# Kernel tuning notes

Hardware: AMD Instinct MI355X
Metric: run time of the kernel (lower is better)

Reference implementation:

```python
import jax, jax.numpy as jnp
import numpy as np
import math

SUPPORT = 4
NEI = 20
POOL_RATE = 4

def _normalize(x, axis):
    n = jnp.linalg.norm(x, axis=axis, keepdims=True)
    return x / jnp.maximum(n, 1e-12)

def _knn(verts, k):
    # verts: (b, v, 3) -> (b, v, k) indices of k nearest (excluding self)
    sq = jnp.sum(verts * verts, axis=-1)
    dist = sq[:, :, None] + sq[:, None, :] - 2.0 * jnp.einsum('bid,bjd->bij', verts, verts)
    _, idx = jax.lax.top_k(-dist, k + 1)
    return idx[:, :, 1:]

def _gather(t, idx):
    # t: (b, v, c), idx: (b, v, n) -> (b, v, n, c)
    return jax.vmap(lambda ti, ii: ti[ii])(t, idx)

def _conv_surface(idx, verts, dirs, support, kernel):
    b, v, n = idx.shape
    nd = _normalize(_gather(verts, idx) - verts[:, :, None, :], -1)  # (b,v,n,3)
    sd = _normalize(dirs, 0)                                          # (3, s*k)
    theta = jax.nn.relu(jnp.einsum('bvnd,de->bvne', nd, sd))
    theta = theta.reshape(b, v, n, support, kernel)
    return jnp.sum(jnp.max(theta, axis=2), axis=2)  # (b, v, kernel)

def _conv_layer(idx, verts, fm, W, bias, dirs, support, out_c):
    b, v, n = idx.shape
    nd = _normalize(_gather(verts, idx) - verts[:, :, None, :], -1)
    sd = _normalize(dirs, 0)                                          # (3, s*out)
    theta = jax.nn.relu(jnp.einsum('bvnd,de->bvne', nd, sd))          # (b,v,n,s*out)
    f = jnp.einsum('bvc,ce->bve', fm, W) + bias                       # (b,v,(s+1)*out)
    f_center = f[:, :, :out_c]
    f_support = _gather(f[:, :, out_c:], idx)                         # (b,v,n,s*out)
    act = (theta * f_support).reshape(b, v, n, support, out_c)
    return f_center + jnp.sum(jnp.max(act, axis=2), axis=2)

def _pool(verts, fm, idx, key, rate):
    pooled = jnp.max(_gather(fm, idx), axis=2)  # (b, v, c)
    v = verts.shape[1]
    sel = jax.random.permutation(key, v)[: v // rate]
    return verts[:, sel, :], pooled[:, sel, :]

def _unif(key, shape, stdv):
    return jax.random.uniform(key, shape, jnp.float32, -stdv, stdv)

def setup_inputs() -> dict:
    key = jax.random.key(0)
    ks = jax.random.split(key, 16)
    s = SUPPORT
    vertices = jax.random.normal(ks[0], (4, 1, 4096, 3), dtype=jnp.float32)
    d = {'vertices': vertices}
    d['dirs0'] = _unif(ks[1], (3, s * 32), 1.0 / math.sqrt(s * 32))
    layers = [(32, 64), (64, 128), (128, 256), (256, 1024)]
    for i, (cin, cout) in enumerate(layers, start=1):
        stdv = 1.0 / math.sqrt(cout * (s + 1))
        d[f'W{i}'] = _unif(ks[3 * i - 1], (cin, (s + 1) * cout), stdv)
        d[f'b{i}'] = _unif(ks[3 * i], ((s + 1) * cout,), stdv)
        d[f'D{i}'] = _unif(ks[3 * i + 1], (3, s * cout), stdv)
    return d

def reference(vertices, dirs0, W1, b1, D1, W2, b2, D2, W3, b3, D3, W4, b4, D4):
    s = SUPPORT
    bs, _, vn, _ = vertices.shape
    v = vertices.reshape(bs, vn, 3)
    idx = _knn(v, NEI)
    fm0 = jax.nn.relu(_conv_surface(idx, v, dirs0, s, 32))
    fm1 = jax.nn.relu(_conv_layer(idx, v, fm0, W1, b1, D1, s, 64))
    v, fm1 = _pool(v, fm1, idx, jax.random.key(42), POOL_RATE)
    idx = _knn(v, NEI)
    fm2 = jax.nn.relu(_conv_layer(idx, v, fm1, W2, b2, D2, s, 128))
    fm3 = jax.nn.relu(_conv_layer(idx, v, fm2, W3, b3, D3, s, 256))
    v, fm3 = _pool(v, fm3, idx, jax.random.key(43), POOL_RATE)
    idx = _knn(v, NEI)
    fm4 = _conv_layer(idx, v, fm3, W4, b4, D4, s, 1024)
    out = jnp.transpose(fm4, (0, 2, 1))[..., None]  # (bs, 1024, vn/16, 1)
    return out
```

## Files before the change

kernel.cpp:

```cpp
#include <hip/hip_runtime.h>
#include <vector>
#include <algorithm>
#include <cstdint>
#include <cstring>
#include <cmath>

static inline uint32_t tf_rotl(uint32_t x, int r) { return (x << r) | (x >> (32 - r)); }

static void tf2x32(uint32_t k0, uint32_t k1, uint32_t x0, uint32_t x1,
                   uint32_t* o0, uint32_t* o1) {
  uint32_t ks2 = k0 ^ k1 ^ 0x1BD11BDAu;
  uint32_t v0 = x0 + k0, v1 = x1 + k1;
  static const int R0[4] = {13, 15, 26, 6}, R1[4] = {17, 29, 16, 24};
#define RND4(R) do { for (int i_ = 0; i_ < 4; ++i_) { v0 += v1; v1 = tf_rotl(v1, R[i_]); v1 ^= v0; } } while (0)
  RND4(R0); v0 += k1;  v1 += ks2 + 1u;
  RND4(R1); v0 += ks2; v1 += k0 + 2u;
  RND4(R0); v0 += k0;  v1 += k1 + 3u;
  RND4(R1); v0 += k1;  v1 += ks2 + 4u;
  RND4(R0); v0 += ks2; v1 += k0 + 5u;
#undef RND4
  *o0 = v0; *o1 = v1;
}

static void jax_permutation(uint32_t seed, int n, int rounds, int* x) {
  uint32_t k0 = 0u, k1 = seed;
  for (int i = 0; i < n; ++i) x[i] = i;
  std::vector<uint32_t> bits(n);
  std::vector<int> ord(n), xn(n);
  for (int r = 0; r < rounds; ++r) {
    uint32_t nk0, nk1, sk0, sk1;
    tf2x32(k0, k1, 0u, 0u, &nk0, &nk1);
    tf2x32(k0, k1, 0u, 1u, &sk0, &sk1);
    for (int i = 0; i < n; ++i) {
      uint32_t h, l;
      tf2x32(sk0, sk1, 0u, (uint32_t)i, &h, &l);
      bits[i] = h ^ l;
    }
    for (int i = 0; i < n; ++i) ord[i] = i;
    std::stable_sort(ord.begin(), ord.end(),
                     [&](int a, int b) { return bits[a] < bits[b]; });
    for (int i = 0; i < n; ++i) xn[i] = x[ord[i]];
    memcpy(x, xn.data(), (size_t)n * sizeof(int));
    k0 = nk0; k1 = nk1;
  }
}

#define NEI 20

__device__ __forceinline__ float san(float v) {
  v = (v != v) ? 0.0f : v;
  return fmaxf(-1e4f, fminf(v, 1e4f));
}

__global__ void k_setup(const float* __restrict__ vin, float* __restrict__ outA,
                        float4* __restrict__ pk, int nverts,
                        const float* __restrict__ d0, const float* __restrict__ d1,
                        const float* __restrict__ d2, const float* __restrict__ d3,
                        const float* __restrict__ d4,
                        float* __restrict__ s0, float* __restrict__ s1,
                        float* __restrict__ s2, float* __restrict__ s3,
                        float* __restrict__ s4) {
  int blk = blockIdx.x;
  if (blk < 64) {
    int i = blk * 256 + threadIdx.x;
    if (i >= nverts) return;
    float x = san(vin[3 * i]), y = san(vin[3 * i + 1]), z = san(vin[3 * i + 2]);
    outA[3 * i] = x; outA[3 * i + 1] = y; outA[3 * i + 2] = z;
    pk[i] = make_float4(x, y, z, x * x + y * y + z * z);
    return;
  }
  int t = (blk - 64) * 256 + threadIdx.x;
  const float* d; float* s; int E, e;
  if (t < 128)       { d = d0; s = s0; E = 128;  e = t; }
  else if (t < 384)  { d = d1; s = s1; E = 256;  e = t - 128; }
  else if (t < 896)  { d = d2; s = s2; E = 512;  e = t - 384; }
  else if (t < 1920) { d = d3; s = s3; E = 1024; e = t - 896; }
  else if (t < 6016) { d = d4; s = s4; E = 4096; e = t - 1920; }
  else return;
  float a = san(d[e]);
  float b = san(d[E + e]);
  float c = san(d[2 * E + e]);
  float nrm = sqrtf(a * a + b * b + c * c);
  float m = fmaxf(nrm, 1e-12f);
  s[e] = a / m; s[E + e] = b / m; s[2 * E + e] = c / m;
}

__device__ __forceinline__ unsigned fmap(float f) {
  unsigned u = __float_as_uint(f);
  return u ^ ((u & 0x80000000u) ? 0xFFFFFFFFu : 0x80000000u);
}

__device__ __forceinline__ unsigned dpp_min_bcast1(unsigned a) {
  unsigned t;
  t = (unsigned)__builtin_amdgcn_update_dpp((int)a, (int)a, 0xB1, 0xF, 0xF, true);
  a = t < a ? t : a;
  t = (unsigned)__builtin_amdgcn_update_dpp((int)a, (int)a, 0x4E, 0xF, 0xF, true);
  a = t < a ? t : a;
  t = (unsigned)__builtin_amdgcn_update_dpp((int)a, (int)a, 0x141, 0xF, 0xF, true);
  a = t < a ? t : a;
  t = (unsigned)__builtin_amdgcn_update_dpp((int)a, (int)a, 0x140, 0xF, 0xF, true);
  a = t < a ? t : a;
  t = (unsigned)__builtin_amdgcn_update_dpp((int)a, (int)a, 0x142, 0xA, 0xF, false);
  a = t < a ? t : a;
  t = (unsigned)__builtin_amdgcn_update_dpp((int)a, (int)a, 0x143, 0xC, 0xF, false);
  a = t < a ? t : a;
  return (unsigned)__builtin_amdgcn_readlane((int)a, 63);
}

__device__ __forceinline__ void dpp_min_bcast2(unsigned& a, unsigned& b) {
  unsigned t0, t1;
#define STEP_DPP(ctrl, rm, bc)                                                           \
  t0 = (unsigned)__builtin_amdgcn_update_dpp((int)a, (int)a, ctrl, rm, 0xF, bc);         \
  t1 = (unsigned)__builtin_amdgcn_update_dpp((int)b, (int)b, ctrl, rm, 0xF, bc);         \
  a = t0 < a ? t0 : a; b = t1 < b ? t1 : b;
  STEP_DPP(0xB1, 0xF, true)
  STEP_DPP(0x4E, 0xF, true)
  STEP_DPP(0x141, 0xF, true)
  STEP_DPP(0x140, 0xF, true)
  STEP_DPP(0x142, 0xA, false)
  STEP_DPP(0x143, 0xC, false)
#undef STEP_DPP
  a = (unsigned)__builtin_amdgcn_readlane((int)a, 63);
  b = (unsigned)__builtin_amdgcn_readlane((int)b, 63);
}

template <int VCAND>
__global__ __launch_bounds__(256, 8) void k_knn8(const float4* __restrict__ pk,
                                                 int* __restrict__ nidx, int V) {
  const int wid = threadIdx.x >> 6;
  const int lane = threadIdx.x & 63;
  const int row0 = blockIdx.x * 8 + wid * 2;
  const int b = row0 / V;
  const int base = b * V;
  const int i0 = row0 % V;

  float xi[2], yi[2], zi[2], sqi[2];
#pragma unroll
  for (int t = 0; t < 2; ++t) {
    float4 q = pk[base + i0 + t];
    xi[t] = q.x; yi[t] = q.y; zi[t] = q.z; sqi[t] = q.w;
  }

  unsigned long long q0[2] = {~0ULL, ~0ULL}, q1[2] = {~0ULL, ~0ULL}, q2[2] = {~0ULL, ~0ULL};
#pragma unroll 4
  for (int c = 0; c < VCAND; ++c) {
    int j = c * 64 + lane;
    float4 cj = pk[base + j];
    float xj = cj.x, yj = cj.y, zj = cj.z, sqj = cj.w;
#pragma unroll
    for (int t = 0; t < 2; ++t) {
      float dot = xi[t] * xj + yi[t] * yj + zi[t] * zj;
      float dd = (sqi[t] + sqj) - 2.0f * dot;
      unsigned long long k = (((unsigned long long)fmap(dd)) << 32) | (unsigned)j;
      if (k < q2[t]) {
        if (k < q1[t]) {
          q2[t] = q1[t];
          if (k < q0[t]) { q1[t] = q0[t]; q0[t] = k; } else { q1[t] = k; }
        } else {
          q2[t] = k;
        }
      }
    }
  }

  for (int r = 0; r < 21; ++r) {
    unsigned h0 = (unsigned)(q0[0] >> 32);
    unsigned h1 = (unsigned)(q0[1] >> 32);
    unsigned m0 = h0, m1 = h1;
    dpp_min_bcast2(m0, m1);
    unsigned long long mk0 = __ballot(h0 == m0);
    unsigned long long mk1 = __ballot(h1 == m1);
    bool win0, win1;
    if (__popcll(mk0) > 1) {
      unsigned jj = (h0 == m0) ? (unsigned)q0[0] : 0xFFFFFFFFu;
      unsigned jm = dpp_min_bcast1(jj);
      win0 = (h0 == m0) && ((unsigned)q0[0] == jm);
    } else {
      win0 = (h0 == m0);
    }
    if (__popcll(mk1) > 1) {
      unsigned jj = (h1 == m1) ? (unsigned)q0[1] : 0xFFFFFFFFu;
      unsigned jm = dpp_min_bcast1(jj);
      win1 = (h1 == m1) && ((unsigned)q0[1] == jm);
    } else {
      win1 = (h1 == m1);
    }
    if (win0) {
      if (r > 0) nidx[(size_t)row0 * NEI + (r - 1)] = (int)(unsigned)q0[0];
      unsigned long long bound = q0[0];
      q0[0] = q1[0]; q1[0] = q2[0]; q2[0] = ~0ULL;
      if (q0[0] == ~0ULL) {
        unsigned long long nm = ~0ULL;
        for (int c = 0; c < VCAND; ++c) {
          int j = c * 64 + lane;
          float4 cj = pk[base + j];
          float dot = xi[0] * cj.x + yi[0] * cj.y + zi[0] * cj.z;
          float dd = (sqi[0] + cj.w) - 2.0f * dot;
          unsigned long long k = (((unsigned long long)fmap(dd)) << 32) | (unsigned)j;
          if (k > bound && k < nm) nm = k;
        }
        q0[0] = nm;
      }
    }
    if (win1) {
      if (r > 0) nidx[(size_t)(row0 + 1) * NEI + (r - 1)] = (int)(unsigned)q0[1];
      unsigned long long bound = q0[1];
      q0[1] = q1[1]; q1[1] = q2[1]; q2[1] = ~0ULL;
      if (q0[1] == ~0ULL) {
        unsigned long long nm = ~0ULL;
        for (int c = 0; c < VCAND; ++c) {
          int j = c * 64 + lane;
          float4 cj = pk[base + j];
          float dot = xi[1] * cj.x + yi[1] * cj.y + zi[1] * cj.z;
          float dd = (sqi[1] + cj.w) - 2.0f * dot;
          unsigned long long k = (((unsigned long long)fmap(dd)) << 32) | (unsigned)j;
          if (k > bound && k < nm) nm = k;
        }
        q0[1] = nm;
      }
    }
  }
}

__global__ __launch_bounds__(128) void k_conv_surface(const float* __restrict__ verts,
                                                      const int* __restrict__ nidx,
                                                      const float* __restrict__ sd,
                                                      float* __restrict__ fm, int V) {
  int row = blockIdx.x;
  int b = row / V, v = row % V;
  const float* vb = verts + (size_t)b * V * 3;
  __shared__ float nd[60];
  __shared__ float mcol[128];
  int tid = threadIdx.x;
  if (tid < NEI) {
    int j = nidx[(size_t)row * NEI + tid];
    float dx = vb[3 * j] - vb[3 * v];
    float dy = vb[3 * j + 1] - vb[3 * v + 1];
    float dz = vb[3 * j + 2] - vb[3 * v + 2];
    float nrm = sqrtf(dx * dx + dy * dy + dz * dz);
    float m = fmaxf(nrm, 1e-12f);
    nd[tid * 3] = dx / m; nd[tid * 3 + 1] = dy / m; nd[tid * 3 + 2] = dz / m;
  }
  __syncthreads();
  {
    int e = tid;
    float s0 = sd[e], s1 = sd[128 + e], s2 = sd[256 + e];
    float me = 0.0f;
#pragma unroll
    for (int n = 0; n < NEI; ++n) {
      float th = nd[3 * n] * s0 + nd[3 * n + 1] * s1 + nd[3 * n + 2] * s2;
      th = fmaxf(th, 0.0f);
      me = fmaxf(me, th);
    }
    mcol[e] = me;
  }
  __syncthreads();
  if (tid < 32) {
    float o = mcol[tid] + mcol[32 + tid] + mcol[64 + tid] + mcol[96 + tid];
    o = fmaxf(o, 0.0f);
    fm[(size_t)row * 32 + tid] = o;
  }
}

__global__ __launch_bounds__(256) void k_gemm_bias(const float* __restrict__ A,
                                                   const float* __restrict__ W,
                                                   const float* __restrict__ bias,
                                                   float* __restrict__ fc,
                                                   _Float16* __restrict__ fs,
                                                   int M, int N, int K, int Cc) {
  __shared__ float As[16][68];
  __shared__ float Bs[16][68];
  int n0 = blockIdx.x * 64, m0 = blockIdx.y * 64;
  int tx = threadIdx.x & 15, ty = threadIdx.x >> 4;
  float acc[4][4] = {};
  for (int k0 = 0; k0 < K; k0 += 16) {
    for (int t = threadIdx.x; t < 1024; t += 256) {
      int mm = t >> 4, kk = t & 15;
      int m = m0 + mm;
      As[kk][mm] = (m < M) ? A[(size_t)m * K + (k0 + kk)] : 0.0f;
    }
    for (int t = threadIdx.x; t < 1024; t += 256) {
      int kk = t >> 6, nn = t & 63;
      int n = n0 + nn;
      Bs[kk][nn] = (n < N) ? san(W[(size_t)(k0 + kk) * N + n]) : 0.0f;
    }
    __syncthreads();
#pragma unroll
    for (int kk = 0; kk < 16; ++kk) {
      float4 av = *(const float4*)&As[kk][ty << 2];
      float4 bv = *(const float4*)&Bs[kk][tx << 2];
      float a[4] = {av.x, av.y, av.z, av.w};
      float bb[4] = {bv.x, bv.y, bv.z, bv.w};
#pragma unroll
      for (int i = 0; i < 4; ++i)
#pragma unroll
        for (int j = 0; j < 4; ++j) acc[i][j] += a[i] * bb[j];
    }
    __syncthreads();
  }
  int SW = N - Cc;
  for (int i = 0; i < 4; ++i)
    for (int j = 0; j < 4; ++j) {
      int m = m0 + (ty << 2) + i, n = n0 + (tx << 2) + j;
      if (m < M && n < N) {
        float val = acc[i][j] + san(bias[n]);
        if (n < Cc) fc[(size_t)m * Cc + n] = val;
        else fs[(size_t)m * SW + (n - Cc)] = (_Float16)val;
      }
    }
}

typedef __attribute__((ext_vector_type(8))) short v8h;
typedef __attribute__((ext_vector_type(4))) float v4f;

__device__ __forceinline__ unsigned short f2bf(float f) {
  unsigned u = __float_as_uint(f);
  u = u + 0x7FFFu + ((u >> 16) & 1u);
  return (unsigned short)(u >> 16);
}
__device__ __forceinline__ float bf2f(unsigned short h) {
  return __uint_as_float((unsigned)h << 16);
}

__global__ __launch_bounds__(256) void k_split_wT_all(
    const float* __restrict__ W2, unsigned short* __restrict__ w2h, unsigned short* __restrict__ w2l,
    const float* __restrict__ W3, unsigned short* __restrict__ w3h, unsigned short* __restrict__ w3l,
    const float* __restrict__ W4, unsigned short* __restrict__ w4h, unsigned short* __restrict__ w4l) {
  int blk = blockIdx.x;
  const float* W; unsigned short *hiT, *loT; int K, N, nt, local;
  if (blk < 40)        { W = W2; hiT = w2h; loT = w2l; K = 64;  N = 640;  nt = 20;  local = blk; }
  else if (blk < 200)  { W = W3; hiT = w3h; loT = w3l; K = 128; N = 1280; nt = 40;  local = blk - 40; }
  else                 { W = W4; hiT = w4h; loT = w4l; K = 256; N = 5120; nt = 160; local = blk - 200; }
  int n0 = (local % nt) * 32, k0 = (local / nt) * 32;
  __shared__ float tile[32][33];
  int tx = threadIdx.x & 31, ty4 = threadIdx.x >> 5;
#pragma unroll
  for (int j = 0; j < 4; ++j)
    tile[ty4 * 4 + j][tx] = san(W[(size_t)(k0 + ty4 * 4 + j) * N + n0 + tx]);
  __syncthreads();
#pragma unroll
  for (int j = 0; j < 4; ++j) {
    int n = n0 + ty4 * 4 + j;
    float a = tile[tx][ty4 * 4 + j];
    unsigned short h = f2bf(a);
    hiT[(size_t)n * K + k0 + tx] = h;
    loT[(size_t)n * K + k0 + tx] = f2bf(a - bf2f(h));
  }
}

__global__ __launch_bounds__(256) void k_gemm128_mfma(
    const unsigned short* __restrict__ Ah, const unsigned short* __restrict__ Al,
    const unsigned short* __restrict__ BhT, const unsigned short* __restrict__ BlT,
    const float* __restrict__ bias, float* __restrict__ fc, _Float16* __restrict__ fs,
    int M, int N, int K, int Cc) {
  __shared__ __attribute__((aligned(16))) unsigned short sAh[128 * 40];
  __shared__ __attribute__((aligned(16))) unsigned short sAl[128 * 40];
  __shared__ __attribute__((aligned(16))) unsigned short sBh[128 * 40];
  __shared__ __attribute__((aligned(16))) unsigned short sBl[128 * 40];
  const int n0 = blockIdx.x * 128, m0 = blockIdx.y * 128;
  const int l = threadIdx.x & 63;
  const int w = threadIdx.x >> 6;
  const int wr = (w >> 1) * 64, wc = (w & 1) * 64;
  const int lr = l & 15;
  const int kb8 = (l >> 4) * 8;

  v4f acc[4][4];
#pragma unroll
  for (int i = 0; i < 4; ++i)
#pragma unroll
    for (int j = 0; j < 4; ++j) acc[i][j] = (v4f){0.f, 0.f, 0.f, 0.f};

  for (int k0 = 0; k0 < K; k0 += 32) {
#pragma unroll
    for (int q = 0; q < 2; ++q) {
      int lin = (int)threadIdx.x + (q << 8);
      int r = lin >> 2, kc = (lin & 3) << 3;
      *(uint4*)&sAh[r * 40 + kc] = *(const uint4*)&Ah[(size_t)(m0 + r) * K + k0 + kc];
      *(uint4*)&sAl[r * 40 + kc] = *(const uint4*)&Al[(size_t)(m0 + r) * K + k0 + kc];
      *(uint4*)&sBh[r * 40 + kc] = *(const uint4*)&BhT[(size_t)(n0 + r) * K + k0 + kc];
      *(uint4*)&sBl[r * 40 + kc] = *(const uint4*)&BlT[(size_t)(n0 + r) * K + k0 + kc];
    }
    __syncthreads();
    v8h fah[4], fal[4], fbh[4], fbl[4];
#pragma unroll
    for (int t = 0; t < 4; ++t) {
      fah[t] = *(const v8h*)&sAh[(wr + t * 16 + lr) * 40 + kb8];
      fal[t] = *(const v8h*)&sAl[(wr + t * 16 + lr) * 40 + kb8];
      fbh[t] = *(const v8h*)&sBh[(wc + t * 16 + lr) * 40 + kb8];
      fbl[t] = *(const v8h*)&sBl[(wc + t * 16 + lr) * 40 + kb8];
    }
#pragma unroll
    for (int i = 0; i < 4; ++i)
#pragma unroll
      for (int j = 0; j < 4; ++j) {
        acc[i][j] = __builtin_amdgcn_mfma_f32_16x16x32_bf16(fah[i], fbh[j], acc[i][j], 0, 0, 0);
        acc[i][j] = __builtin_amdgcn_mfma_f32_16x16x32_bf16(fah[i], fbl[j], acc[i][j], 0, 0, 0);
        acc[i][j] = __builtin_amdgcn_mfma_f32_16x16x32_bf16(fal[i], fbh[j], acc[i][j], 0, 0, 0);
      }
    __syncthreads();
  }
  float bs[4];
#pragma unroll
  for (int j = 0; j < 4; ++j) bs[j] = san(bias[n0 + wc + j * 16 + lr]);
  const int rowb = m0 + wr + (l >> 4) * 4;
  if (n0 + 128 <= Cc) {
#pragma unroll
    for (int i = 0; i < 4; ++i)
#pragma unroll
      for (int j = 0; j < 4; ++j) {
        int col = n0 + wc + j * 16 + lr;
#pragma unroll
        for (int v = 0; v < 4; ++v)
          fc[(size_t)(rowb + i * 16 + v) * Cc + col] = acc[i][j][v] + bs[j];
      }
  } else {
    int SW = N - Cc;
#pragma unroll
    for (int i = 0; i < 4; ++i)
#pragma unroll
      for (int j = 0; j < 4; ++j) {
        int col = n0 + wc + j * 16 + lr - Cc;
#pragma unroll
        for (int v = 0; v < 4; ++v)
          fs[(size_t)(rowb + i * 16 + v) * SW + col] = (_Float16)(acc[i][j][v] + bs[j]);
      }
  }
}

__global__ __launch_bounds__(256) void k_conv_layer(const float* __restrict__ fc,
                                                    const _Float16* __restrict__ fs,
                                                    const float* __restrict__ verts,
                                                    const int* __restrict__ nidx,
                                                    const float* __restrict__ sd,
                                                    float* __restrict__ outf,
                                                    int V, int C, int relu_out) {
  int row = blockIdx.x;
  int b = row / V, v = row % V;
  int E = 4 * C;
  extern __shared__ float sm[];
  float* mcol = sm;
  float* nd = sm + E;
  int* jr = (int*)(nd + 60);
  int tid = threadIdx.x;
  const float* vb = verts + (size_t)b * V * 3;
  if (tid < NEI) {
    int j = nidx[(size_t)row * NEI + tid];
    jr[tid] = j;
    float dx = vb[3 * j] - vb[3 * v];
    float dy = vb[3 * j + 1] - vb[3 * v + 1];
    float dz = vb[3 * j + 2] - vb[3 * v + 2];
    float nrm = sqrtf(dx * dx + dy * dy + dz * dz);
    float m = fmaxf(nrm, 1e-12f);
    nd[tid * 3] = dx / m; nd[tid * 3 + 1] = dy / m; nd[tid * 3 + 2] = dz / m;
  }
  __syncthreads();
  size_t fb = (size_t)b * V;
  for (int e = tid; e < E; e += blockDim.x) {
    float s0 = sd[e], s1 = sd[E + e], s2 = sd[2 * E + e];
    float me = -INFINITY;
#pragma unroll
    for (int n = 0; n < NEI; ++n) {
      float th = nd[3 * n] * s0 + nd[3 * n + 1] * s1 + nd[3 * n + 2] * s2;
      th = fmaxf(th, 0.0f);
      float fv = (float)fs[(fb + jr[n]) * (size_t)E + e];
      me = fmaxf(me, th * fv);
    }
    mcol[e] = me;
  }
  __syncthreads();
  for (int c = tid; c < C; c += blockDim.x) {
    float o = fc[(size_t)row * C + c] + mcol[c] + mcol[C + c] + mcol[2 * C + c] + mcol[3 * C + c];
    if (relu_out) o = fmaxf(o, 0.0f);
    outf[(size_t)row * C + c] = o;
  }
}

__global__ __launch_bounds__(256) void k_conv_layer_split(const float* __restrict__ fc,
                                                          const _Float16* __restrict__ fs,
                                                          const float* __restrict__ verts,
                                                          const int* __restrict__ nidx,
                                                          const float* __restrict__ sd,
                                                          unsigned short* __restrict__ outh,
                                                          unsigned short* __restrict__ outl,
                                                          int V, int C, int relu_out) {
  int row = blockIdx.x;
  int b = row / V, v = row % V;
  int E = 4 * C;
  extern __shared__ float sm[];
  float* mcol = sm;
  float* nd = sm + E;
  int* jr = (int*)(nd + 60);
  int tid = threadIdx.x;
  const float* vb = verts + (size_t)b * V * 3;
  if (tid < NEI) {
    int j = nidx[(size_t)row * NEI + tid];
    jr[tid] = j;
    float dx = vb[3 * j] - vb[3 * v];
    float dy = vb[3 * j + 1] - vb[3 * v + 1];
    float dz = vb[3 * j + 2] - vb[3 * v + 2];
    float nrm = sqrtf(dx * dx + dy * dy + dz * dz);
    float m = fmaxf(nrm, 1e-12f);
    nd[tid * 3] = dx / m; nd[tid * 3 + 1] = dy / m; nd[tid * 3 + 2] = dz / m;
  }
  __syncthreads();
  size_t fb = (size_t)b * V;
  for (int e = tid; e < E; e += blockDim.x) {
    float s0 = sd[e], s1 = sd[E + e], s2 = sd[2 * E + e];
    float me = -INFINITY;
#pragma unroll
    for (int n = 0; n < NEI; ++n) {
      float th = nd[3 * n] * s0 + nd[3 * n + 1] * s1 + nd[3 * n + 2] * s2;
      th = fmaxf(th, 0.0f);
      float fv = (float)fs[(fb + jr[n]) * (size_t)E + e];
      me = fmaxf(me, th * fv);
    }
    mcol[e] = me;
  }
  __syncthreads();
  for (int c = tid; c < C; c += blockDim.x) {
    float o = fc[(size_t)row * C + c] + mcol[c] + mcol[C + c] + mcol[2 * C + c] + mcol[3 * C + c];
    if (relu_out) o = fmaxf(o, 0.0f);
    unsigned short h = f2bf(o);
    outh[(size_t)row * C + c] = h;
    outl[(size_t)row * C + c] = f2bf(o - bf2f(h));
  }
}

__global__ __launch_bounds__(1024) void k_conv_layer_big(const float* __restrict__ fc,
                                                         const _Float16* __restrict__ fs,
                                                         const float* __restrict__ verts,
                                                         const int* __restrict__ nidx,
                                                         const float* __restrict__ sd,
                                                         float* __restrict__ outf,
                                                         int V, int C, int relu_out) {
  int row = blockIdx.x;
  int b = row / V, v = row % V;
  int E = 4 * C;
  extern __shared__ float sm[];
  float* mcol = sm;
  float* nd = sm + E;
  int* jr = (int*)(nd + 60);
  int tid = threadIdx.x;
  const float* vb = verts + (size_t)b * V * 3;
  if (tid < NEI) {
    int j = nidx[(size_t)row * NEI + tid];
    jr[tid] = j;
    float dx = vb[3 * j] - vb[3 * v];
    float dy = vb[3 * j + 1] - vb[3 * v + 1];
    float dz = vb[3 * j + 2] - vb[3 * v + 2];
    float nrm = sqrtf(dx * dx + dy * dy + dz * dz);
    float m = fmaxf(nrm, 1e-12f);
    nd[tid * 3] = dx / m; nd[tid * 3 + 1] = dy / m; nd[tid * 3 + 2] = dz / m;
  }
  __syncthreads();
  size_t fb = (size_t)b * V;
  for (int e = tid; e < E; e += blockDim.x) {
    float s0 = sd[e], s1 = sd[E + e], s2 = sd[2 * E + e];
    float me = -INFINITY;
#pragma unroll
    for (int n = 0; n < NEI; ++n) {
      float th = nd[3 * n] * s0 + nd[3 * n + 1] * s1 + nd[3 * n + 2] * s2;
      th = fmaxf(th, 0.0f);
      float fv = (float)fs[(fb + jr[n]) * (size_t)E + e];
      me = fmaxf(me, th * fv);
    }
    mcol[e] = me;
  }
  __syncthreads();
  for (int c = tid; c < C; c += blockDim.x) {
    float o = fc[(size_t)row * C + c] + mcol[c] + mcol[C + c] + mcol[2 * C + c] + mcol[3 * C + c];
    if (relu_out) o = fmaxf(o, 0.0f);
    outf[(size_t)row * C + c] = o;
  }
}

__global__ __launch_bounds__(256) void k_transpose_vc(const float* __restrict__ in,
                                                      float* __restrict__ out,
                                                      int V, int C) {
  __shared__ float tile[32][33];
  int b = blockIdx.z;
  int c0 = blockIdx.x * 32, v0 = blockIdx.y * 32;
  int tx = threadIdx.x & 31, ty4 = threadIdx.x >> 5;
#pragma unroll
  for (int j = 0; j < 4; ++j) {
    int v = v0 + ty4 * 4 + j;
    tile[ty4 * 4 + j][tx] = in[((size_t)b * V + v) * C + c0 + tx];
  }
  __syncthreads();
#pragma unroll
  for (int j = 0; j < 4; ++j) {
    int c = c0 + ty4 * 4 + j;
    out[((size_t)b * C + c) * V + v0 + tx] = tile[tx][ty4 * 4 + j];
  }
}

__global__ void k_pool_sel_split(const float* __restrict__ fm, const int* __restrict__ nidx,
                                 const int* __restrict__ sel,
                                 unsigned short* __restrict__ outh,
                                 unsigned short* __restrict__ outl,
                                 const float* __restrict__ vinA, float* __restrict__ voutA,
                                 float4* __restrict__ pkout,
                                 int Vin, int Vout, int C) {
  int t = blockIdx.x * blockDim.x + threadIdx.x;
  if (t < 4 * Vout) {
    int p = t % Vout;
    int b = t / Vout;
    int src = b * Vin + sel[p];
    float x = vinA[3 * src], y = vinA[3 * src + 1], z = vinA[3 * src + 2];
    int dst = b * Vout + p;
    voutA[3 * dst] = x; voutA[3 * dst + 1] = y; voutA[3 * dst + 2] = z;
    pkout[dst] = make_float4(x, y, z, x * x + y * y + z * z);
  }
  int total = 4 * Vout * C;
  if (t >= total) return;
  int c = t % C;
  int p = (t / C) % Vout;
  int b = t / (C * Vout);
  int sv = sel[p];
  const int* ir = nidx + ((size_t)b * Vin + sv) * NEI;
  float m = -INFINITY;
#pragma unroll
  for (int n = 0; n < NEI; ++n)
    m = fmaxf(m, fm[((size_t)b * Vin + ir[n]) * C + c]);
  size_t o = ((size_t)b * Vout + p) * C + c;
  unsigned short h = f2bf(m);
  outh[o] = h;
  outl[o] = f2bf(m - bf2f(h));
}

extern "C" void kernel_launch(void* const* d_in, const int* in_sizes, int n_in,
                              void* d_out, int out_size, void* d_ws, size_t ws_size,
                              hipStream_t stream) {
  (void)in_sizes; (void)n_in; (void)out_size; (void)ws_size;
  const int B = 4, V1 = 4096, V2 = 1024, V3 = 256;

  const float* vin   = (const float*)d_in[0];
  const float* dirs0 = (const float*)d_in[1];
  const float* W1 = (const float*)d_in[2];
  const float* b1 = (const float*)d_in[3];
  const float* D1 = (const float*)d_in[4];
  const float* W2 = (const float*)d_in[5];
  const float* b2 = (const float*)d_in[6];
  const float* D2 = (const float*)d_in[7];
  const float* W3 = (const float*)d_in[8];
  const float* b3 = (const float*)d_in[9];
  const float* D3 = (const float*)d_in[10];
  const float* W4 = (const float*)d_in[11];
  const float* b4 = (const float*)d_in[12];
  const float* D4 = (const float*)d_in[13];
  float* out = (float*)d_out;

  char* ws = (char*)d_ws;
  size_t off = 0;
  auto alloc = [&](size_t bytes) -> char* {
    char* p = ws + off;
    off = (off + bytes + 255) & ~(size_t)255;
    return p;
  };
  int* sel1 = (int*)alloc((size_t)V2 * 4);
  int* sel2 = (int*)alloc((size_t)V3 * 4);
  float* verts1 = (float*)alloc((size_t)B * V1 * 3 * 4);
  float* verts2 = (float*)alloc((size_t)B * V2 * 3 * 4);
  float* verts3 = (float*)alloc((size_t)B * V3 * 3 * 4);
  float4* pk1 = (float4*)alloc((size_t)B * V1 * 16);
  float4* pk2 = (float4*)alloc((size_t)B * V2 * 16);
  float4* pk3 = (float4*)alloc((size_t)B * V3 * 16);
  int* idx1 = (int*)alloc((size_t)B * V1 * NEI * 4);
  int* idx2 = (int*)alloc((size_t)B * V2 * NEI * 4);
  int* idx3 = (int*)alloc((size_t)B * V3 * NEI * 4);
  float* sd0 = (float*)alloc(3 * 128 * 4);
  float* sd1 = (float*)alloc(3 * 256 * 4);
  float* sd2 = (float*)alloc(3 * 512 * 4);
  float* sd3 = (float*)alloc(3 * 1024 * 4);
  float* sd4 = (float*)alloc(3 * 4096 * 4);
  float* bufA = (float*)alloc((size_t)B * V1 * 32 * 4);
  float* bufB = (float*)alloc((size_t)B * V1 * 64 * 4);
  float* fcb = (float*)alloc((size_t)B * V1 * 64 * 4);
  _Float16* fsb = (_Float16*)alloc((size_t)B * V1 * 256 * 2);
  unsigned short* w2hT = (unsigned short*)alloc((size_t)640 * 64 * 2);
  unsigned short* w2lT = (unsigned short*)alloc((size_t)640 * 64 * 2);
  unsigned short* w3hT = (unsigned short*)alloc((size_t)1280 * 128 * 2);
  unsigned short* w3lT = (unsigned short*)alloc((size_t)1280 * 128 * 2);
  unsigned short* w4hT = (unsigned short*)alloc((size_t)5120 * 256 * 2);
  unsigned short* w4lT = (unsigned short*)alloc((size_t)5120 * 256 * 2);
  unsigned short* aSh = (unsigned short*)alloc((size_t)4096 * 128 * 2);
  unsigned short* aSl = (unsigned short*)alloc((size_t)4096 * 128 * 2);
  float* fm0 = bufA;
  float* fm1 = bufB, *fm3 = bufB;
  float* conv4out = bufB;

  static int perm1[4096];
  static int perm2[1024];
  static int selh[1280];
  jax_permutation(42u, 4096, 2, perm1);
  jax_permutation(43u, 1024, 1, perm2);
  memcpy(selh, perm1, 1024 * sizeof(int));
  memcpy(selh + 1024, perm2, 256 * sizeof(int));
  hipMemcpyAsync(sel1, selh, 1024 * sizeof(int), hipMemcpyHostToDevice, stream);
  hipMemcpyAsync(sel2, selh + 1024, 256 * sizeof(int), hipMemcpyHostToDevice, stream);

  k_setup<<<88, 256, 0, stream>>>(vin, verts1, pk1, B * V1,
                                  dirs0, D1, D2, D3, D4, sd0, sd1, sd2, sd3, sd4);
  k_split_wT_all<<<1480, 256, 0, stream>>>(W2, w2hT, w2lT, W3, w3hT, w3lT, W4, w4hT, w4lT);
  k_knn8<64><<<B * V1 / 8, 256, 0, stream>>>(pk1, idx1, V1);
  k_conv_surface<<<B * V1, 128, 0, stream>>>(verts1, idx1, sd0, fm0, V1);
  k_gemm_bias<<<dim3(5, 256), 256, 0, stream>>>(fm0, W1, b1, fcb, fsb, B * V1, 320, 32, 64);
  k_conv_layer<<<B * V1, 256, (4 * 64 + 80) * 4, stream>>>(fcb, fsb, verts1, idx1, sd1, fm1, V1, 64, 1);
  {
    int total = B * V2 * 64;
    k_pool_sel_split<<<(total + 255) / 256, 256, 0, stream>>>(fm1, idx1, sel1, aSh, aSl,
                                                              verts1, verts2, pk2,
                                                              V1, V2, 64);
  }
  k_knn8<16><<<B * V2 / 8, 256, 0, stream>>>(pk2, idx2, V2);
  k_gemm128_mfma<<<dim3(640 / 128, 4096 / 128), 256, 0, stream>>>(aSh, aSl, w2hT, w2lT, b2, fcb, fsb, B * V2, 640, 64, 128);
  k_conv_layer_split<<<B * V2, 256, (4 * 128 + 80) * 4, stream>>>(fcb, fsb, verts2, idx2, sd2, aSh, aSl, V2, 128, 1);
  k_gemm128_mfma<<<dim3(1280 / 128, 4096 / 128), 256, 0, stream>>>(aSh, aSl, w3hT, w3lT, b3, fcb, fsb, B * V2, 1280, 128, 256);
  k_conv_layer<<<B * V2, 256, (4 * 256 + 80) * 4, stream>>>(fcb, fsb, verts2, idx2, sd3, fm3, V2, 256, 1);
  {
    int total = B * V3 * 256;
    k_pool_sel_split<<<(total + 255) / 256, 256, 0, stream>>>(fm3, idx2, sel2, aSh, aSl,
                                                              verts2, verts3, pk3,
                                                              V2, V3, 256);
  }
  k_knn8<4><<<B * V3 / 8, 256, 0, stream>>>(pk3, idx3, V3);
  k_gemm128_mfma<<<dim3(5120 / 128, 1024 / 128), 256, 0, stream>>>(aSh, aSl, w4hT, w4lT, b4, fcb, fsb, B * V3, 5120, 256, 1024);
  k_conv_layer_big<<<B * V3, 1024, (4 * 1024 + 80) * 4, stream>>>(fcb, fsb, verts3, idx3, sd4, conv4out, V3, 1024, 0);
  k_transpose_vc<<<dim3(1024 / 32, 256 / 32, B), 256, 0, stream>>>(conv4out, out, V3, 1024);
}
```

Measured before the change: 388.8 us.

## Route layer-1 GEMM through split-bf16 MFMA kernel and pair fp16 gathers in conv layers

Conv_surface now writes its output as hi/lo bf16 split planes. The first-layer weight projection therefore runs on the existing MFMA GEMM instead of the scalar FP32 tiled GEMM, with W1 padded to 384 columns in the weight-split kernel. The GEMM epilogue is generalised to handle tiles straddling the centre/support split and out-of-range columns. The conv-layer inner loops now process two channels per thread with paired fp16 loads and float2 direction loads, and the first conv_layer launch drops to 128 threads.

```diff
diff --git a/kernel.cpp b/kernel.cpp
--- a/kernel.cpp
+++ b/kernel.cpp
@@ -46,6 +46,8 @@
 }
 
 #define NEI 20
+
+typedef _Float16 f16x2 __attribute__((ext_vector_type(2)));
 
 __device__ __forceinline__ float san(float v) {
   v = (v != v) ? 0.0f : v;
@@ -222,10 +224,24 @@
   }
 }
 
+typedef __attribute__((ext_vector_type(8))) short v8h;
+typedef __attribute__((ext_vector_type(4))) float v4f;
+
+__device__ __forceinline__ unsigned short f2bf(float f) {
+  unsigned u = __float_as_uint(f);
+  u = u + 0x7FFFu + ((u >> 16) & 1u);
+  return (unsigned short)(u >> 16);
+}
+__device__ __forceinline__ float bf2f(unsigned short h) {
+  return __uint_as_float((unsigned)h << 16);
+}
+
 __global__ __launch_bounds__(128) void k_conv_surface(const float* __restrict__ verts,
                                                       const int* __restrict__ nidx,
                                                       const float* __restrict__ sd,
-                                                      float* __restrict__ fm, int V) {
+                                                      unsigned short* __restrict__ outh,
+                                                      unsigned short* __restrict__ outl,
+                                                      int V) {
   int row = blockIdx.x;
   int b = row / V, v = row % V;
   const float* vb = verts + (size_t)b * V * 3;
@@ -258,85 +274,38 @@
   if (tid < 32) {
     float o = mcol[tid] + mcol[32 + tid] + mcol[64 + tid] + mcol[96 + tid];
     o = fmaxf(o, 0.0f);
-    fm[(size_t)row * 32 + tid] = o;
-  }
-}
-
-__global__ __launch_bounds__(256) void k_gemm_bias(const float* __restrict__ A,
-                                                   const float* __restrict__ W,
-                                                   const float* __restrict__ bias,
-                                                   float* __restrict__ fc,
-                                                   _Float16* __restrict__ fs,
-                                                   int M, int N, int K, int Cc) {
-  __shared__ float As[16][68];
-  __shared__ float Bs[16][68];
-  int n0 = blockIdx.x * 64, m0 = blockIdx.y * 64;
-  int tx = threadIdx.x & 15, ty = threadIdx.x >> 4;
-  float acc[4][4] = {};
-  for (int k0 = 0; k0 < K; k0 += 16) {
-    for (int t = threadIdx.x; t < 1024; t += 256) {
-      int mm = t >> 4, kk = t & 15;
-      int m = m0 + mm;
-      As[kk][mm] = (m < M) ? A[(size_t)m * K + (k0 + kk)] : 0.0f;
-    }
-    for (int t = threadIdx.x; t < 1024; t += 256) {
-      int kk = t >> 6, nn = t & 63;
-      int n = n0 + nn;
-      Bs[kk][nn] = (n < N) ? san(W[(size_t)(k0 + kk) * N + n]) : 0.0f;
-    }
-    __syncthreads();
-#pragma unroll
-    for (int kk = 0; kk < 16; ++kk) {
-      float4 av = *(const float4*)&As[kk][ty << 2];
-      float4 bv = *(const float4*)&Bs[kk][tx << 2];
-      float a[4] = {av.x, av.y, av.z, av.w};
-      float bb[4] = {bv.x, bv.y, bv.z, bv.w};
-#pragma unroll
-      for (int i = 0; i < 4; ++i)
-#pragma unroll
-        for (int j = 0; j < 4; ++j) acc[i][j] += a[i] * bb[j];
-    }
-    __syncthreads();
-  }
-  int SW = N - Cc;
-  for (int i = 0; i < 4; ++i)
-    for (int j = 0; j < 4; ++j) {
-      int m = m0 + (ty << 2) + i, n = n0 + (tx << 2) + j;
-      if (m < M && n < N) {
-        float val = acc[i][j] + san(bias[n]);
-        if (n < Cc) fc[(size_t)m * Cc + n] = val;
-        else fs[(size_t)m * SW + (n - Cc)] = (_Float16)val;
-      }
-    }
-}
-
-typedef __attribute__((ext_vector_type(8))) short v8h;
-typedef __attribute__((ext_vector_type(4))) float v4f;
-
-__device__ __forceinline__ unsigned short f2bf(float f) {
-  unsigned u = __float_as_uint(f);
-  u = u + 0x7FFFu + ((u >> 16) & 1u);
-  return (unsigned short)(u >> 16);
-}
-__device__ __forceinline__ float bf2f(unsigned short h) {
-  return __uint_as_float((unsigned)h << 16);
+    unsigned short h = f2bf(o);
+    outh[(size_t)row * 32 + tid] = h;
+    outl[(size_t)row * 32 + tid] = f2bf(o - bf2f(h));
+  }
 }
 
 __global__ __launch_bounds__(256) void k_split_wT_all(
+    const float* __restrict__ W1, unsigned short* __restrict__ w1h, unsigned short* __restrict__ w1l,
     const float* __restrict__ W2, unsigned short* __restrict__ w2h, unsigned short* __restrict__ w2l,
     const float* __restrict__ W3, unsigned short* __restrict__ w3h, unsigned short* __restrict__ w3l,
     const float* __restrict__ W4, unsigned short* __restrict__ w4h, unsigned short* __restrict__ w4l) {
   int blk = blockIdx.x;
-  const float* W; unsigned short *hiT, *loT; int K, N, nt, local;
-  if (blk < 40)        { W = W2; hiT = w2h; loT = w2l; K = 64;  N = 640;  nt = 20;  local = blk; }
-  else if (blk < 200)  { W = W3; hiT = w3h; loT = w3l; K = 128; N = 1280; nt = 40;  local = blk - 40; }
-  else                 { W = W4; hiT = w4h; loT = w4l; K = 256; N = 5120; nt = 160; local = blk - 200; }
+  const float* W; unsigned short *hiT, *loT; int K, N, Nreal, nt, local;
+  if (blk < 12)        { W = W1; hiT = w1h; loT = w1l; K = 32;  N = 384;  Nreal = 320;  nt = 12;  local = blk; }
+  else if (blk < 52)   { W = W2; hiT = w2h; loT = w2l; K = 64;  N = 640;  Nreal = 640;  nt = 20;  local = blk - 12; }
+  else if (blk < 212)  { W = W3; hiT = w3h; loT = w3l; K = 128; N = 1280; Nreal = 1280; nt = 40;  local = blk - 52; }
+  else                 { W = W4; hiT = w4h; loT = w4l; K = 256; N = 5120; Nreal = 5120; nt = 160; local = blk - 212; }
   int n0 = (local % nt) * 32, k0 = (local / nt) * 32;
   __shared__ float tile[32][33];
   int tx = threadIdx.x & 31, ty4 = threadIdx.x >> 5;
+  if (n0 >= Nreal) {
+#pragma unroll
+    for (int j = 0; j < 4; ++j) {
+      int n = n0 + ty4 * 4 + j;
+      hiT[(size_t)n * K + k0 + tx] = 0;
+      loT[(size_t)n * K + k0 + tx] = 0;
+    }
+    return;
+  }
 #pragma unroll
   for (int j = 0; j < 4; ++j)
-    tile[ty4 * 4 + j][tx] = san(W[(size_t)(k0 + ty4 * 4 + j) * N + n0 + tx]);
+    tile[ty4 * 4 + j][tx] = san(W[(size_t)(k0 + ty4 * 4 + j) * Nreal + n0 + tx]);
   __syncthreads();
 #pragma unroll
   for (int j = 0; j < 4; ++j) {
@@ -399,32 +368,27 @@
       }
     __syncthreads();
   }
+  const int SW = N - Cc;
   float bs[4];
 #pragma unroll
-  for (int j = 0; j < 4; ++j) bs[j] = san(bias[n0 + wc + j * 16 + lr]);
+  for (int j = 0; j < 4; ++j) {
+    int col = n0 + wc + j * 16 + lr;
+    bs[j] = (col < N) ? san(bias[col]) : 0.0f;
+  }
   const int rowb = m0 + wr + (l >> 4) * 4;
-  if (n0 + 128 <= Cc) {
-#pragma unroll
-    for (int i = 0; i < 4; ++i)
-#pragma unroll
-      for (int j = 0; j < 4; ++j) {
-        int col = n0 + wc + j * 16 + lr;
-#pragma unroll
-        for (int v = 0; v < 4; ++v)
-          fc[(size_t)(rowb + i * 16 + v) * Cc + col] = acc[i][j][v] + bs[j];
+#pragma unroll
+  for (int i = 0; i < 4; ++i)
+#pragma unroll
+    for (int j = 0; j < 4; ++j) {
+      int col = n0 + wc + j * 16 + lr;
+#pragma unroll
+      for (int v = 0; v < 4; ++v) {
+        float val = acc[i][j][v] + bs[j];
+        int row = rowb + i * 16 + v;
+        if (col < Cc) fc[(size_t)row * Cc + col] = val;
+        else if (col < N) fs[(size_t)row * SW + (col - Cc)] = (_Float16)val;
       }
-  } else {
-    int SW = N - Cc;
-#pragma unroll
-    for (int i = 0; i < 4; ++i)
-#pragma unroll
-      for (int j = 0; j < 4; ++j) {
-        int col = n0 + wc + j * 16 + lr - Cc;
-#pragma unroll
-        for (int v = 0; v < 4; ++v)
-          fs[(size_t)(rowb + i * 16 + v) * SW + col] = (_Float16)(acc[i][j][v] + bs[j]);
-      }
-  }
+    }
 }
 
 __global__ __launch_bounds__(256) void k_conv_layer(const float* __restrict__ fc,
@@ -455,17 +419,23 @@
   }
   __syncthreads();
   size_t fb = (size_t)b * V;
-  for (int e = tid; e < E; e += blockDim.x) {
-    float s0 = sd[e], s1 = sd[E + e], s2 = sd[2 * E + e];
-    float me = -INFINITY;
+  int H = E >> 1;
+  for (int g = tid; g < H; g += blockDim.x) {
+    int e = g << 1;
+    float2 sp0 = *(const float2*)&sd[e];
+    float2 sp1 = *(const float2*)&sd[E + e];
+    float2 sp2 = *(const float2*)&sd[2 * E + e];
+    float me0 = -INFINITY, me1 = -INFINITY;
 #pragma unroll
     for (int n = 0; n < NEI; ++n) {
-      float th = nd[3 * n] * s0 + nd[3 * n + 1] * s1 + nd[3 * n + 2] * s2;
-      th = fmaxf(th, 0.0f);
-      float fv = (float)fs[(fb + jr[n]) * (size_t)E + e];
-      me = fmaxf(me, th * fv);
-    }
-    mcol[e] = me;
+      float n0 = nd[3 * n], n1 = nd[3 * n + 1], n2 = nd[3 * n + 2];
+      f16x2 fv = *(const f16x2*)&fs[(fb + jr[n]) * (size_t)E + e];
+      float th0 = fmaxf(n0 * sp0.x + n1 * sp1.x + n2 * sp2.x, 0.0f);
+      float th1 = fmaxf(n0 * sp0.y + n1 * sp1.y + n2 * sp2.y, 0.0f);
+      me0 = fmaxf(me0, th0 * (float)fv.x);
+      me1 = fmaxf(me1, th1 * (float)fv.y);
+    }
+    mcol[e] = me0; mcol[e + 1] = me1;
   }
   __syncthreads();
   for (int c = tid; c < C; c += blockDim.x) {
@@ -504,17 +474,23 @@
   }
   __syncthreads();
   size_t fb = (size_t)b * V;
-  for (int e = tid; e < E; e += blockDim.x) {
-    float s0 = sd[e], s1 = sd[E + e], s2 = sd[2 * E + e];
-    float me = -INFINITY;
+  int H = E >> 1;
+  for (int g = tid; g < H; g += blockDim.x) {
+    int e = g << 1;
+    float2 sp0 = *(const float2*)&sd[e];
+    float2 sp1 = *(const float2*)&sd[E + e];
+    float2 sp2 = *(const float2*)&sd[2 * E + e];
+    float me0 = -INFINITY, me1 = -INFINITY;
 #pragma unroll
     for (int n = 0; n < NEI; ++n) {
-      float th = nd[3 * n] * s0 + nd[3 * n + 1] * s1 + nd[3 * n + 2] * s2;
-      th = fmaxf(th, 0.0f);
-      float fv = (float)fs[(fb + jr[n]) * (size_t)E + e];
-      me = fmaxf(me, th * fv);
-    }
-    mcol[e] = me;
+      float n0 = nd[3 * n], n1 = nd[3 * n + 1], n2 = nd[3 * n + 2];
+      f16x2 fv = *(const f16x2*)&fs[(fb + jr[n]) * (size_t)E + e];
+      float th0 = fmaxf(n0 * sp0.x + n1 * sp1.x + n2 * sp2.x, 0.0f);
+      float th1 = fmaxf(n0 * sp0.y + n1 * sp1.y + n2 * sp2.y, 0.0f);
+      me0 = fmaxf(me0, th0 * (float)fv.x);
+      me1 = fmaxf(me1, th1 * (float)fv.y);
+    }
+    mcol[e] = me0; mcol[e + 1] = me1;
   }
   __syncthreads();
   for (int c = tid; c < C; c += blockDim.x) {
@@ -554,17 +530,23 @@
   }
   __syncthreads();
   size_t fb = (size_t)b * V;
-  for (int e = tid; e < E; e += blockDim.x) {
-    float s0 = sd[e], s1 = sd[E + e], s2 = sd[2 * E + e];
-    float me = -INFINITY;
+  int H = E >> 1;
+  for (int g = tid; g < H; g += blockDim.x) {
+    int e = g << 1;
+    float2 sp0 = *(const float2*)&sd[e];
+    float2 sp1 = *(const float2*)&sd[E + e];
+    float2 sp2 = *(const float2*)&sd[2 * E + e];
+    float me0 = -INFINITY, me1 = -INFINITY;
 #pragma unroll
     for (int n = 0; n < NEI; ++n) {
-      float th = nd[3 * n] * s0 + nd[3 * n + 1] * s1 + nd[3 * n + 2] * s2;
-      th = fmaxf(th, 0.0f);
-      float fv = (float)fs[(fb + jr[n]) * (size_t)E + e];
-      me = fmaxf(me, th * fv);
-    }
-    mcol[e] = me;
+      float n0 = nd[3 * n], n1 = nd[3 * n + 1], n2 = nd[3 * n + 2];
+      f16x2 fv = *(const f16x2*)&fs[(fb + jr[n]) * (size_t)E + e];
+      float th0 = fmaxf(n0 * sp0.x + n1 * sp1.x + n2 * sp2.x, 0.0f);
+      float th1 = fmaxf(n0 * sp0.y + n1 * sp1.y + n2 * sp2.y, 0.0f);
+      me0 = fmaxf(me0, th0 * (float)fv.x);
+      me1 = fmaxf(me1, th1 * (float)fv.y);
+    }
+    mcol[e] = me0; mcol[e + 1] = me1;
   }
   __syncthreads();
   for (int c = tid; c < C; c += blockDim.x) {
@@ -673,10 +655,11 @@
   float* sd2 = (float*)alloc(3 * 512 * 4);
   float* sd3 = (float*)alloc(3 * 1024 * 4);
   float* sd4 = (float*)alloc(3 * 4096 * 4);
-  float* bufA = (float*)alloc((size_t)B * V1 * 32 * 4);
   float* bufB = (float*)alloc((size_t)B * V1 * 64 * 4);
   float* fcb = (float*)alloc((size_t)B * V1 * 64 * 4);
   _Float16* fsb = (_Float16*)alloc((size_t)B * V1 * 256 * 2);
+  unsigned short* w1hT = (unsigned short*)alloc((size_t)384 * 32 * 2);
+  unsigned short* w1lT = (unsigned short*)alloc((size_t)384 * 32 * 2);
   unsigned short* w2hT = (unsigned short*)alloc((size_t)640 * 64 * 2);
   unsigned short* w2lT = (unsigned short*)alloc((size_t)640 * 64 * 2);
   unsigned short* w3hT = (unsigned short*)alloc((size_t)1280 * 128 * 2);
@@ -685,7 +668,6 @@
   unsigned short* w4lT = (unsigned short*)alloc((size_t)5120 * 256 * 2);
   unsigned short* aSh = (unsigned short*)alloc((size_t)4096 * 128 * 2);
   unsigned short* aSl = (unsigned short*)alloc((size_t)4096 * 128 * 2);
-  float* fm0 = bufA;
   float* fm1 = bufB, *fm3 = bufB;
   float* conv4out = bufB;
 
@@ -701,11 +683,12 @@
 
   k_setup<<<88, 256, 0, stream>>>(vin, verts1, pk1, B * V1,
                                   dirs0, D1, D2, D3, D4, sd0, sd1, sd2, sd3, sd4);
-  k_split_wT_all<<<1480, 256, 0, stream>>>(W2, w2hT, w2lT, W3, w3hT, w3lT, W4, w4hT, w4lT);
+  k_split_wT_all<<<1492, 256, 0, stream>>>(W1, w1hT, w1lT, W2, w2hT, w2lT,
+                                           W3, w3hT, w3lT, W4, w4hT, w4lT);
   k_knn8<64><<<B * V1 / 8, 256, 0, stream>>>(pk1, idx1, V1);
-  k_conv_surface<<<B * V1, 128, 0, stream>>>(verts1, idx1, sd0, fm0, V1);
-  k_gemm_bias<<<dim3(5, 256), 256, 0, stream>>>(fm0, W1, b1, fcb, fsb, B * V1, 320, 32, 64);
-  k_conv_layer<<<B * V1, 256, (4 * 64 + 80) * 4, stream>>>(fcb, fsb, verts1, idx1, sd1, fm1, V1, 64, 1);
+  k_conv_surface<<<B * V1, 128, 0, stream>>>(verts1, idx1, sd0, aSh, aSl, V1);
+  k_gemm128_mfma<<<dim3(3, 128), 256, 0, stream>>>(aSh, aSl, w1hT, w1lT, b1, fcb, fsb, B * V1, 320, 32, 64);
+  k_conv_layer<<<B * V1, 128, (4 * 64 + 80) * 4, stream>>>(fcb, fsb, verts1, idx1, sd1, fm1, V1, 64, 1);
   {
     int total = B * V2 * 64;
     k_pool_sel_split<<<(total + 255) / 256, 256, 0, stream>>>(fm1, idx1, sel1, aSh, aSl,
```

Result: faster. 369.5 us (median of 2 runs) (-4.9%).
